# Kernel tuning notes

Measured on AMD Instinct MI355X. Metric: run time of the kernel, lower is better.

## Reference

```python
import jax, jax.numpy as jnp
import numpy as np

# Dims: T timesteps, B batch, C channels, HID expert hidden, E experts, K top-k
T, B, C, HID, E, K, H, W = 4, 8, 256, 1024, 8, 2, 14, 14
EPS = 1e-5       # BatchNorm eps
ALPHA = 4.0      # spikingjelly sigmoid surrogate alpha
V_TH = 1.0       # LIF threshold (spikingjelly default), v_reset = 0.0


@jax.custom_vjp
def spike_fn(u):
    # Heaviside forward, sigmoid-surrogate backward (spikingjelly surrogate.Sigmoid)
    return (u >= 0.0).astype(u.dtype)

def _spike_fwd(u):
    return (u >= 0.0).astype(u.dtype), u

def _spike_bwd(u, g):
    s = jax.nn.sigmoid(ALPHA * u)
    return (g * ALPHA * s * (1.0 - s),)

spike_fn.defvjp(_spike_fwd, _spike_bwd)


def lif(x, tau):
    """MultiStepLIFNode with hard reset (v_reset=0), detach_reset=True.
    x: (T, B, C, H, W) -> spikes of same shape."""
    def step(v, xt):
        h = v + (xt - v) / tau                      # charge
        s = spike_fn(h - V_TH)                      # fire
        v_new = h * (1.0 - jax.lax.stop_gradient(s))  # hard reset, detached spike
        return v_new, s
    _, spikes = jax.lax.scan(step, jnp.zeros_like(x[0]), x)
    return spikes


def conv1x1(x, w, b):
    # x: (T,B,Cin,H,W), w: (Cout,Cin), b: (Cout,) -- 1x1 conv == channel GEMM
    return jnp.einsum('tbchw,oc->tbohw', x, w) + b[None, None, :, None, None]


def bn(x, g, b, m, v, axis):
    # inference-mode BatchNorm with running stats, per-channel on `axis`
    shp = [1] * x.ndim
    shp[axis] = -1
    scale = g.reshape(shp) / jnp.sqrt(v.reshape(shp) + EPS)
    return (x - m.reshape(shp)) * scale + b.reshape(shp)


def expert(x, tau, w1, b1, g1, be1, m1, v1, w2, b2, g2, be2, m2, v2):
    # MS_MLP_Expert.forward: lif -> conv1x1 -> bn -> lif -> conv1x1 -> bn (no residual)
    s1 = lif(x, tau)
    h = bn(conv1x1(s1, w1, b1), g1, be1, m1, v1, axis=2)  # (T,B,HID,H,W)
    s2 = lif(h, tau)
    return bn(conv1x1(s2, w2, b2), g2, be2, m2, v2, axis=2)  # (T,B,C,H,W)


def setup_inputs() -> dict:
    key = jax.random.key(0)
    ks = jax.random.split(key, 16)
    d = {}
    d['x'] = jax.random.normal(ks[0], (T, B, C, H, W), jnp.float32)
    # router (Conv2d(C, E, 1) + BatchNorm2d(E))
    d['router_w'] = jax.random.normal(ks[1], (E, C), jnp.float32) / np.sqrt(C)
    d['router_b'] = jax.random.normal(ks[2], (E,), jnp.float32) * 0.01
    d['rbn_g'] = 1.0 + 0.1 * jax.random.normal(ks[3], (E,), jnp.float32)
    d['rbn_b'] = 0.1 * jax.random.normal(ks[4], (E,), jnp.float32)
    d['rbn_m'] = 0.1 * jax.random.normal(ks[5], (E,), jnp.float32)
    d['rbn_v'] = jax.random.uniform(ks[6], (E,), jnp.float32, 0.5, 1.5)
    # stacked expert params (leading expert axis E)
    d['fc1_w'] = jax.random.normal(ks[7], (E, HID, C), jnp.float32) / np.sqrt(C)
    d['fc1_b'] = 0.01 * jax.random.normal(ks[8], (E, HID), jnp.float32)
    d['bn1_g'] = 1.0 + 0.1 * jax.random.normal(ks[9], (E, HID), jnp.float32)
    d['bn1_b'] = 0.1 * jax.random.normal(ks[10], (E, HID), jnp.float32)
    d['bn1_m'] = 0.1 * jax.random.normal(ks[11], (E, HID), jnp.float32)
    d['bn1_v'] = jax.random.uniform(ks[12], (E, HID), jnp.float32, 0.5, 1.5)
    d['fc2_w'] = jax.random.normal(ks[13], (E, C, HID), jnp.float32) / np.sqrt(HID)
    d['fc2_b'] = 0.01 * jax.random.normal(ks[14], (E, C), jnp.float32)
    d['bn2_g'] = 1.0 + 0.1 * jax.random.normal(ks[15], (E, C), jnp.float32)
    k2 = jax.random.split(jax.random.fold_in(key, 1), 3)
    d['bn2_b'] = 0.1 * jax.random.normal(k2[0], (E, C), jnp.float32)
    d['bn2_m'] = 0.1 * jax.random.normal(k2[1], (E, C), jnp.float32)
    d['bn2_v'] = jax.random.uniform(k2[2], (E, C), jnp.float32, 0.5, 1.5)
    # expert taus: linspace(tau_min=1.5, tau_max=4.0, num_experts)
    d['taus'] = jnp.linspace(1.5, 4.0, E, dtype=jnp.float32)
    return d


def reference(x, router_w, router_b, rbn_g, rbn_b, rbn_m, rbn_v,
              fc1_w, fc1_b, bn1_g, bn1_b, bn1_m, bn1_v,
              fc2_w, fc2_b, bn2_g, bn2_b, bn2_m, bn2_v, taus):
    b_sz = x.shape[1]
    # ---- TemporalRouter ----
    xm = x.mean(axis=0)                                           # (B,C,H,W)
    r = jnp.einsum('bchw,ec->behw', xm, router_w) + router_b[None, :, None, None]
    r = bn(r, rbn_g, rbn_b, rbn_m, rbn_v, axis=1)
    logits = r.mean(axis=(-2, -1))                                # (B,E)
    probs = jax.nn.softmax(logits, axis=-1)
    topw, topi = jax.lax.top_k(probs, K)                          # (B,K)
    topw = topw / topw.sum(axis=-1, keepdims=True)
    # dense combine weights (B,E): top-k entries, 0 elsewhere; detached as in torch
    Wd = jnp.zeros((b_sz, E), x.dtype).at[jnp.arange(b_sz)[:, None], topi].add(topw)
    Wd = jax.lax.stop_gradient(Wd)
    # ---- Experts (dense dispatch: each expert over full batch, masked combine) ----
    outs = jax.vmap(expert, in_axes=(None,) + (0,) * 13)(
        x, taus, fc1_w, fc1_b, bn1_g, bn1_b, bn1_m, bn1_v,
        fc2_w, fc2_b, bn2_g, bn2_b, bn2_m, bn2_v)                 # (E,T,B,C,H,W)
    moe = jnp.einsum('etbchw,be->tbchw', outs, Wd)
    return x + moe
```

## Files before the change

kernel.cpp:

```cpp
#include <hip/hip_runtime.h>
#include <hip/hip_bf16.h>
#include <math.h>

#define T_ 4
#define B_ 8
#define C_ 256
#define HID_ 1024
#define E_ 8
#define HW_ 196
#define M_ 784
#define NPAIR_ 16
#define EPS_ 1e-5f
#define NOUT_ (T_*B_*C_*HW_)

typedef __attribute__((ext_vector_type(8))) short bf16x8;
typedef __attribute__((ext_vector_type(4))) unsigned short u16x4;
typedef __attribute__((ext_vector_type(4))) float f32x4;

__device__ inline unsigned short f2bf(float f){
  union { float f; unsigned u; } v; v.f = f;
  unsigned u = v.u;
  unsigned r = u + 0x7FFFu + ((u >> 16) & 1u);
  return (unsigned short)(r >> 16);
}
__device__ inline float bf2f(unsigned short h){
  union { unsigned u; float f; } v; v.u = ((unsigned)h) << 16;
  return v.f;
}

__device__ inline void gl16(const void* g, void* l){
  auto gp = reinterpret_cast<const unsigned int __attribute__((address_space(1)))*>(
      reinterpret_cast<uintptr_t>(g));
  auto lp = reinterpret_cast<unsigned int __attribute__((address_space(3)))*>(
      reinterpret_cast<uintptr_t>(l));
  __builtin_amdgcn_global_load_lds(gp, lp, 16, 0, 0);
}

__global__ __launch_bounds__(256) void wconv_kernel(
    const float* __restrict__ w1, const float* __restrict__ w2,
    unsigned short* __restrict__ w1h, unsigned short* __restrict__ w1l,
    unsigned short* __restrict__ w2h){
  int i = blockIdx.x * 256 + threadIdx.x;
  float4 v = ((const float4*)w1)[i];
  u16x4 h, l;
  h[0]=f2bf(v.x); l[0]=f2bf(v.x - bf2f(h[0]));
  h[1]=f2bf(v.y); l[1]=f2bf(v.y - bf2f(h[1]));
  h[2]=f2bf(v.z); l[2]=f2bf(v.z - bf2f(h[2]));
  h[3]=f2bf(v.w); l[3]=f2bf(v.w - bf2f(h[3]));
  ((u16x4*)w1h)[i] = h; ((u16x4*)w1l)[i] = l;
  float4 u = ((const float4*)w2)[i];
  u16x4 h2;
  h2[0]=f2bf(u.x); h2[1]=f2bf(u.y); h2[2]=f2bf(u.z); h2[3]=f2bf(u.w);
  ((u16x4*)w2h)[i] = h2;
}

__global__ __launch_bounds__(64) void xbar_kernel(const float* __restrict__ x,
                                                  float* __restrict__ xbar){
  int bc = blockIdx.x;
  int l = threadIdx.x;
  float s = 0.f;
  for (int t = 0; t < T_; t++){
    const float* p = x + ((size_t)(t * B_ * C_) + bc) * HW_;
    for (int i = l; i < HW_; i += 64) s += p[i];
  }
  for (int off = 32; off > 0; off >>= 1) s += __shfl_down(s, off, 64);
  if (l == 0) xbar[bc] = s * (1.0f / (T_ * HW_));
}

__global__ __launch_bounds__(64) void router_kernel(const float* __restrict__ xbar,
    const float* __restrict__ rw, const float* __restrict__ rb,
    const float* __restrict__ rg, const float* __restrict__ rbb,
    const float* __restrict__ rm, const float* __restrict__ rv,
    int* __restrict__ sel_e, float* __restrict__ sel_w){
  __shared__ float lg[64];
  const int tid = threadIdx.x;
  const int b = tid >> 3, e = tid & 7;
  float dot = 0.f;
  for (int c = 0; c < C_; c++) dot += xbar[b * C_ + c] * rw[e * C_ + c];
  dot += rb[e];
  float sc = rg[e] / sqrtf(rv[e] + EPS_);
  lg[tid] = (dot - rm[e]) * sc + rbb[e];
  __syncthreads();
  if (e == 0){
    float l[E_], mx = -1e30f;
    for (int i = 0; i < E_; i++){ l[i] = lg[b * 8 + i]; mx = fmaxf(mx, l[i]); }
    float p[E_];
    for (int i = 0; i < E_; i++) p[i] = expf(l[i] - mx);
    int i1 = 0;
    for (int i = 1; i < E_; i++) if (p[i] > p[i1]) i1 = i;
    int i2 = (i1 == 0) ? 1 : 0;
    for (int i = 0; i < E_; i++) if (i != i1 && p[i] > p[i2]) i2 = i;
    float denom = p[i1] + p[i2];
    sel_e[b * 2]     = i1; sel_w[b * 2]     = p[i1] / denom;
    sel_e[b * 2 + 1] = i2; sel_w[b * 2 + 1] = p[i2] / denom;
  }
}

__global__ __launch_bounds__(256) void lif1_kernel(const float* __restrict__ x,
    const int* __restrict__ sel_e, const float* __restrict__ taus,
    unsigned short* __restrict__ s1){
  const int hw = blockIdx.x;
  const int pair = blockIdx.y;
  const int c = threadIdx.x;
  const int b = pair >> 1;
  const float tau = taus[sel_e[pair]];
  float v = 0.f;
  #pragma unroll
  for (int t = 0; t < T_; t++){
    float xv = x[((size_t)(t * B_ + b) * C_ + c) * HW_ + hw];
    float h = v + (xv - v) / tau;
    float s = (h >= 1.0f) ? 1.0f : 0.0f;
    v = h * (1.0f - s);
    s1[((size_t)pair * M_ + hw * 4 + t) * C_ + c] =
        (s > 0.5f) ? (unsigned short)0x3F80 : (unsigned short)0;
  }
}


__global__ __launch_bounds__(256) void g1_kernel(
    const unsigned short* __restrict__ s1,
    const unsigned short* __restrict__ w1h, const unsigned short* __restrict__ w1l,
    const float* __restrict__ fc1_b,
    const float* __restrict__ bn1_g, const float* __restrict__ bn1_b,
    const float* __restrict__ bn1_m, const float* __restrict__ bn1_v,
    const int* __restrict__ sel_e, const float* __restrict__ taus,
    unsigned short* __restrict__ s2)
{
  __shared__ __align__(16) unsigned short lA[4][2048];
  __shared__ __align__(16) unsigned short lBh[4][2048];
  __shared__ __align__(16) unsigned short lBl[4][2048];
  const int nt = blockIdx.x, mt = blockIdx.y, pair = blockIdx.z;
  const int e = sel_e[pair];
  const int m0 = mt * 64, n0 = nt * 64;
  const int tid = threadIdx.x, lane = tid & 63, wv = tid >> 6;
  const int l15 = lane & 15;
  const int koffs = ((((lane >> 4) ^ (l15 & 3) ^ ((l15 >> 2) & 1)) & 3) << 3);
  const int srow = wv * 16 + (lane >> 2);
  const int scol = ((((lane & 3) ^ ((lane >> 2) & 3) ^ ((lane >> 4) & 1)) & 3) << 3);
  int arow = m0 + srow; if (arow > M_ - 1) arow = M_ - 1;
  const unsigned short* aG  = s1  + ((size_t)pair * M_ + arow) * C_ + scol;
  const unsigned short* bhG = w1h + ((size_t)e * HID_ + n0 + srow) * C_ + scol;
  const unsigned short* blG = w1l + ((size_t)e * HID_ + n0 + srow) * C_ + scol;
  const int lb = wv * 512;
  #pragma unroll
  for (int p = 0; p < 3; p++){
    gl16(aG  + p * 32, &lA[p][lb]);
    gl16(bhG + p * 32, &lBh[p][lb]);
    gl16(blG + p * 32, &lBl[p][lb]);
  }
  f32x4 acc[4] = {};
  #pragma unroll
  for (int kk = 0; kk < 8; kk++){
    if (kk < 6)       asm volatile("s_waitcnt vmcnt(6)" ::: "memory");
    else if (kk == 6) asm volatile("s_waitcnt vmcnt(3)" ::: "memory");
    else              asm volatile("s_waitcnt vmcnt(0)" ::: "memory");
    __builtin_amdgcn_s_barrier();
    __builtin_amdgcn_sched_barrier(0);
    const int cur = kk & 3;
    bf16x8 a = *(const bf16x8*)(&lA[cur][(wv * 16 + l15) * 32 + koffs]);
    #pragma unroll
    for (int cb = 0; cb < 4; cb++){
      bf16x8 bh = *(const bf16x8*)(&lBh[cur][(cb * 16 + l15) * 32 + koffs]);
      bf16x8 bl = *(const bf16x8*)(&lBl[cur][(cb * 16 + l15) * 32 + koffs]);
      acc[cb] = __builtin_amdgcn_mfma_f32_16x16x32_bf16(a, bh, acc[cb], 0, 0, 0);
      acc[cb] = __builtin_amdgcn_mfma_f32_16x16x32_bf16(a, bl, acc[cb], 0, 0, 0);
    }
    if (kk < 5){
      const int nb = (kk + 3) & 3;
      gl16(aG  + (kk + 3) * 32, &lA[nb][lb]);
      gl16(bhG + (kk + 3) * 32, &lBh[nb][lb]);
      gl16(blG + (kk + 3) * 32, &lBl[nb][lb]);
    }
  }
  const float tau = taus[e];
  const int rbase = m0 + wv * 16 + ((lane >> 4) << 2);
  if (rbase < M_){
    #pragma unroll
    for (int cb = 0; cb < 4; cb++){
      int col = n0 + cb * 16 + l15;
      int pi = e * HID_ + col;
      float sc = bn1_g[pi] / sqrtf(bn1_v[pi] + EPS_);
      float mm = bn1_m[pi], bb = bn1_b[pi], cbias = fc1_b[pi];
      float v = 0.f;
      #pragma unroll
      for (int t = 0; t < 4; t++){
        float z = acc[cb][t] + cbias;
        float hin = (z - mm) * sc + bb;
        float h = v + (hin - v) / tau;
        float s = (h >= 1.0f) ? 1.0f : 0.0f;
        v = h * (1.0f - s);
        s2[((size_t)pair * M_ + rbase + t) * HID_ + col] =
            (s > 0.5f) ? (unsigned short)0x3F80 : (unsigned short)0;
      }
    }
  }
}

__global__ __launch_bounds__(256) void g2_kernel(
    const unsigned short* __restrict__ s2,
    const unsigned short* __restrict__ w2h,
    const float* __restrict__ fc2_b,
    const float* __restrict__ bn2_g, const float* __restrict__ bn2_b,
    const float* __restrict__ bn2_m, const float* __restrict__ bn2_v,
    const int* __restrict__ sel_e, const float* __restrict__ sel_w,
    float* __restrict__ y)
{
  __shared__ __align__(16) unsigned short lA[4][2048];
  __shared__ __align__(16) unsigned short lBh[4][2048];
  const int nt = blockIdx.x, mt = blockIdx.y, pair = blockIdx.z;
  const int e = sel_e[pair];
  const float wgt = sel_w[pair];
  const int b = pair >> 1, slot = pair & 1;
  const int m0 = mt * 64, n0 = nt * 64;
  const int tid = threadIdx.x, lane = tid & 63, wv = tid >> 6;
  const int l15 = lane & 15;
  const int koffs = ((((lane >> 4) ^ (l15 & 3) ^ ((l15 >> 2) & 1)) & 3) << 3);
  const int srow = wv * 16 + (lane >> 2);
  const int scol = ((((lane & 3) ^ ((lane >> 2) & 3) ^ ((lane >> 4) & 1)) & 3) << 3);
  int arow = m0 + srow; if (arow > M_ - 1) arow = M_ - 1;
  const unsigned short* aG  = s2  + ((size_t)pair * M_ + arow) * HID_ + scol;
  const unsigned short* bhG = w2h + ((size_t)e * C_ + n0 + srow) * HID_ + scol;
  const int lb = wv * 512;
  #pragma unroll
  for (int p = 0; p < 3; p++){
    gl16(aG  + p * 32, &lA[p][lb]);
    gl16(bhG + p * 32, &lBh[p][lb]);
  }
  f32x4 acc[4] = {};
  #pragma unroll
  for (int kk = 0; kk < 32; kk++){
    if (kk < 30)       asm volatile("s_waitcnt vmcnt(4)" ::: "memory");
    else if (kk == 30) asm volatile("s_waitcnt vmcnt(2)" ::: "memory");
    else               asm volatile("s_waitcnt vmcnt(0)" ::: "memory");
    __builtin_amdgcn_s_barrier();
    __builtin_amdgcn_sched_barrier(0);
    const int cur = kk & 3;
    bf16x8 a = *(const bf16x8*)(&lA[cur][(wv * 16 + l15) * 32 + koffs]);
    #pragma unroll
    for (int cb = 0; cb < 4; cb++){
      bf16x8 bh = *(const bf16x8*)(&lBh[cur][(cb * 16 + l15) * 32 + koffs]);
      acc[cb] = __builtin_amdgcn_mfma_f32_16x16x32_bf16(a, bh, acc[cb], 0, 0, 0);
    }
    if (kk < 29){
      const int nb = (kk + 3) & 3;
      gl16(aG  + (kk + 3) * 32, &lA[nb][lb]);
      gl16(bhG + (kk + 3) * 32, &lBh[nb][lb]);
    }
  }
  const int rbase = m0 + wv * 16 + ((lane >> 4) << 2);
  if (rbase < M_){
    const int hw = rbase >> 2;
    #pragma unroll
    for (int cb = 0; cb < 4; cb++){
      int col = n0 + cb * 16 + l15;
      int pi = e * C_ + col;
      float sc = bn2_g[pi] / sqrtf(bn2_v[pi] + EPS_);
      float mm = bn2_m[pi], bb = bn2_b[pi], cbias = fc2_b[pi];
      #pragma unroll
      for (int t = 0; t < 4; t++){
        float z = acc[cb][t] + cbias;
        float yv = (z - mm) * sc + bb;
        y[(((size_t)slot * T_ + t) * B_ + b) * (C_ * HW_) + (size_t)col * HW_ + hw] =
            wgt * yv;
      }
    }
  }
}

__global__ __launch_bounds__(256) void combine_kernel(const float* __restrict__ x,
    const float* __restrict__ y, float* __restrict__ out){
  int i = blockIdx.x * 256 + threadIdx.x;
  float4 a  = ((const float4*)x)[i];
  float4 b0 = ((const float4*)y)[i];
  float4 b1 = ((const float4*)y)[i + NOUT_ / 4];
  float4 r;
  r.x = a.x + b0.x + b1.x;
  r.y = a.y + b0.y + b1.y;
  r.z = a.z + b0.z + b1.z;
  r.w = a.w + b0.w + b1.w;
  ((float4*)out)[i] = r;
}

extern "C" void kernel_launch(void* const* d_in, const int* in_sizes, int n_in,
                              void* d_out, int out_size, void* d_ws, size_t ws_size,
                              hipStream_t stream){
  const float* x     = (const float*)d_in[0];
  const float* rw    = (const float*)d_in[1];
  const float* rb    = (const float*)d_in[2];
  const float* rg    = (const float*)d_in[3];
  const float* rbb   = (const float*)d_in[4];
  const float* rm    = (const float*)d_in[5];
  const float* rv    = (const float*)d_in[6];
  const float* fc1_w = (const float*)d_in[7];
  const float* fc1_b = (const float*)d_in[8];
  const float* bn1_g = (const float*)d_in[9];
  const float* bn1_b = (const float*)d_in[10];
  const float* bn1_m = (const float*)d_in[11];
  const float* bn1_v = (const float*)d_in[12];
  const float* fc2_w = (const float*)d_in[13];
  const float* fc2_b = (const float*)d_in[14];
  const float* bn2_g = (const float*)d_in[15];
  const float* bn2_b = (const float*)d_in[16];
  const float* bn2_m = (const float*)d_in[17];
  const float* bn2_v = (const float*)d_in[18];
  const float* taus  = (const float*)d_in[19];
  float* out = (float*)d_out;

  char* ws = (char*)d_ws;
  size_t off = 0;
  auto alloc = [&](size_t bytes) -> char* {
    char* p = ws + off;
    off = (off + bytes + 255) & ~(size_t)255;
    return p;
  };
  const int NW = E_ * HID_ * C_;
  unsigned short* s2  = (unsigned short*)alloc((size_t)NPAIR_ * M_ * HID_ * 2);
  unsigned short* w2h = (unsigned short*)alloc((size_t)NW * 2);
  unsigned short* w1h = (unsigned short*)alloc((size_t)NW * 2);
  unsigned short* w1l = (unsigned short*)alloc((size_t)NW * 2);
  unsigned short* s1  = (unsigned short*)alloc((size_t)NPAIR_ * M_ * C_ * 2);
  float* xbar  = (float*)alloc(B_ * C_ * 4);
  int*   sel_e = (int*)alloc(NPAIR_ * 4);
  float* sel_w = (float*)alloc(NPAIR_ * 4);
  float* y = (float*)w1h;
  (void)ws_size; (void)in_sizes; (void)n_in; (void)out_size;

  wconv_kernel<<<NW / 4 / 256, 256, 0, stream>>>(fc1_w, fc2_w, w1h, w1l, w2h);
  xbar_kernel<<<B_ * C_, 64, 0, stream>>>(x, xbar);
  router_kernel<<<1, 64, 0, stream>>>(xbar, rw, rb, rg, rbb, rm, rv, sel_e, sel_w);
  lif1_kernel<<<dim3(HW_, NPAIR_), 256, 0, stream>>>(x, sel_e, taus, s1);
  g1_kernel<<<dim3(HID_ / 64, (M_ + 63) / 64, NPAIR_), 256, 0, stream>>>(
      s1, w1h, w1l, fc1_b, bn1_g, bn1_b, bn1_m, bn1_v, sel_e, taus, s2);
  g2_kernel<<<dim3(C_ / 64, (M_ + 63) / 64, NPAIR_), 256, 0, stream>>>(
      s2, w2h, fc2_b, bn2_g, bn2_b, bn2_m, bn2_v, sel_e, sel_w, y);
  combine_kernel<<<NOUT_ / 4 / 256, 256, 0, stream>>>(x, y, out);
}
```

Baseline: 197.8 us.

## Fuse expert combine and residual into g2, merge prep kernels, coalesce LIF1

```diff
diff --git a/kernel.cpp b/kernel.cpp
--- a/kernel.cpp
+++ b/kernel.cpp
@@ -36,35 +36,38 @@
   __builtin_amdgcn_global_load_lds(gp, lp, 16, 0, 0);
 }
 
-__global__ __launch_bounds__(256) void wconv_kernel(
+__global__ __launch_bounds__(256) void prep_kernel(
     const float* __restrict__ w1, const float* __restrict__ w2,
+    const float* __restrict__ x,
     unsigned short* __restrict__ w1h, unsigned short* __restrict__ w1l,
-    unsigned short* __restrict__ w2h){
-  int i = blockIdx.x * 256 + threadIdx.x;
-  float4 v = ((const float4*)w1)[i];
-  u16x4 h, l;
-  h[0]=f2bf(v.x); l[0]=f2bf(v.x - bf2f(h[0]));
-  h[1]=f2bf(v.y); l[1]=f2bf(v.y - bf2f(h[1]));
-  h[2]=f2bf(v.z); l[2]=f2bf(v.z - bf2f(h[2]));
-  h[3]=f2bf(v.w); l[3]=f2bf(v.w - bf2f(h[3]));
-  ((u16x4*)w1h)[i] = h; ((u16x4*)w1l)[i] = l;
-  float4 u = ((const float4*)w2)[i];
-  u16x4 h2;
-  h2[0]=f2bf(u.x); h2[1]=f2bf(u.y); h2[2]=f2bf(u.z); h2[3]=f2bf(u.w);
-  ((u16x4*)w2h)[i] = h2;
-}
-
-__global__ __launch_bounds__(64) void xbar_kernel(const float* __restrict__ x,
-                                                  float* __restrict__ xbar){
-  int bc = blockIdx.x;
-  int l = threadIdx.x;
-  float s = 0.f;
-  for (int t = 0; t < T_; t++){
-    const float* p = x + ((size_t)(t * B_ * C_) + bc) * HW_;
-    for (int i = l; i < HW_; i += 64) s += p[i];
-  }
-  for (int off = 32; off > 0; off >>= 1) s += __shfl_down(s, off, 64);
-  if (l == 0) xbar[bc] = s * (1.0f / (T_ * HW_));
+    unsigned short* __restrict__ w2h, float* __restrict__ xbar){
+  const int blk = blockIdx.x;
+  if (blk < 2048){
+    int i = blk * 256 + threadIdx.x;
+    float4 v = ((const float4*)w1)[i];
+    u16x4 h, l;
+    h[0]=f2bf(v.x); l[0]=f2bf(v.x - bf2f(h[0]));
+    h[1]=f2bf(v.y); l[1]=f2bf(v.y - bf2f(h[1]));
+    h[2]=f2bf(v.z); l[2]=f2bf(v.z - bf2f(h[2]));
+    h[3]=f2bf(v.w); l[3]=f2bf(v.w - bf2f(h[3]));
+    ((u16x4*)w1h)[i] = h; ((u16x4*)w1l)[i] = l;
+    float4 u = ((const float4*)w2)[i];
+    u16x4 h2;
+    h2[0]=f2bf(u.x); h2[1]=f2bf(u.y); h2[2]=f2bf(u.z); h2[3]=f2bf(u.w);
+    ((u16x4*)w2h)[i] = h2;
+  } else {
+    const int q = blk - 2048;
+    const int g = threadIdx.x >> 6;
+    const int lane = threadIdx.x & 63;
+    const int bc = q * 4 + g;
+    float s = 0.f;
+    for (int t = 0; t < T_; t++){
+      const float* p = x + ((size_t)(t * B_ * C_) + bc) * HW_;
+      for (int i = lane; i < HW_; i += 64) s += p[i];
+    }
+    for (int off = 32; off > 0; off >>= 1) s += __shfl_down(s, off, 64);
+    if (lane == 0) xbar[bc] = s * (1.0f / (T_ * HW_));
+  }
 }
 
 __global__ __launch_bounds__(64) void router_kernel(const float* __restrict__ xbar,
@@ -99,20 +102,20 @@
 __global__ __launch_bounds__(256) void lif1_kernel(const float* __restrict__ x,
     const int* __restrict__ sel_e, const float* __restrict__ taus,
     unsigned short* __restrict__ s1){
-  const int hw = blockIdx.x;
   const int pair = blockIdx.y;
-  const int c = threadIdx.x;
   const int b = pair >> 1;
+  const int f = blockIdx.x * 256 + threadIdx.x;
+  const int c = f / HW_, hw = f - c * HW_;
   const float tau = taus[sel_e[pair]];
+  unsigned short* o = s1 + (size_t)pair * (M_ * C_) + (size_t)(hw * 4) * C_ + c;
   float v = 0.f;
   #pragma unroll
   for (int t = 0; t < T_; t++){
-    float xv = x[((size_t)(t * B_ + b) * C_ + c) * HW_ + hw];
+    float xv = x[(size_t)(t * B_ + b) * (C_ * HW_) + f];
     float h = v + (xv - v) / tau;
     float s = (h >= 1.0f) ? 1.0f : 0.0f;
     v = h * (1.0f - s);
-    s1[((size_t)pair * M_ + hw * 4 + t) * C_ + c] =
-        (s > 0.5f) ? (unsigned short)0x3F80 : (unsigned short)0;
+    o[t * C_] = (s > 0.5f) ? (unsigned short)0x3F80 : (unsigned short)0;
   }
 }
 
@@ -203,14 +206,11 @@
     const float* __restrict__ bn2_g, const float* __restrict__ bn2_b,
     const float* __restrict__ bn2_m, const float* __restrict__ bn2_v,
     const int* __restrict__ sel_e, const float* __restrict__ sel_w,
-    float* __restrict__ y)
+    const float* __restrict__ x, float* __restrict__ out)
 {
   __shared__ __align__(16) unsigned short lA[4][2048];
   __shared__ __align__(16) unsigned short lBh[4][2048];
-  const int nt = blockIdx.x, mt = blockIdx.y, pair = blockIdx.z;
-  const int e = sel_e[pair];
-  const float wgt = sel_w[pair];
-  const int b = pair >> 1, slot = pair & 1;
+  const int nt = blockIdx.x, mt = blockIdx.y, b = blockIdx.z;
   const int m0 = mt * 64, n0 = nt * 64;
   const int tid = threadIdx.x, lane = tid & 63, wv = tid >> 6;
   const int l15 = lane & 15;
@@ -218,38 +218,40 @@
   const int srow = wv * 16 + (lane >> 2);
   const int scol = ((((lane & 3) ^ ((lane >> 2) & 3) ^ ((lane >> 4) & 1)) & 3) << 3);
   int arow = m0 + srow; if (arow > M_ - 1) arow = M_ - 1;
-  const unsigned short* aG  = s2  + ((size_t)pair * M_ + arow) * HID_ + scol;
-  const unsigned short* bhG = w2h + ((size_t)e * C_ + n0 + srow) * HID_ + scol;
   const int lb = wv * 512;
-  #pragma unroll
-  for (int p = 0; p < 3; p++){
-    gl16(aG  + p * 32, &lA[p][lb]);
-    gl16(bhG + p * 32, &lBh[p][lb]);
-  }
-  f32x4 acc[4] = {};
-  #pragma unroll
-  for (int kk = 0; kk < 32; kk++){
-    if (kk < 30)       asm volatile("s_waitcnt vmcnt(4)" ::: "memory");
-    else if (kk == 30) asm volatile("s_waitcnt vmcnt(2)" ::: "memory");
-    else               asm volatile("s_waitcnt vmcnt(0)" ::: "memory");
-    __builtin_amdgcn_s_barrier();
-    __builtin_amdgcn_sched_barrier(0);
-    const int cur = kk & 3;
-    bf16x8 a = *(const bf16x8*)(&lA[cur][(wv * 16 + l15) * 32 + koffs]);
-    #pragma unroll
-    for (int cb = 0; cb < 4; cb++){
-      bf16x8 bh = *(const bf16x8*)(&lBh[cur][(cb * 16 + l15) * 32 + koffs]);
-      acc[cb] = __builtin_amdgcn_mfma_f32_16x16x32_bf16(a, bh, acc[cb], 0, 0, 0);
-    }
-    if (kk < 29){
-      const int nb = (kk + 3) & 3;
-      gl16(aG  + (kk + 3) * 32, &lA[nb][lb]);
-      gl16(bhG + (kk + 3) * 32, &lBh[nb][lb]);
-    }
-  }
-  const int rbase = m0 + wv * 16 + ((lane >> 4) << 2);
-  if (rbase < M_){
-    const int hw = rbase >> 2;
+  f32x4 res[4] = {};
+  for (int slot = 0; slot < 2; slot++){
+    const int pair = b * 2 + slot;
+    const int e = sel_e[pair];
+    const float wgt = sel_w[pair];
+    const unsigned short* aG  = s2  + ((size_t)pair * M_ + arow) * HID_ + scol;
+    const unsigned short* bhG = w2h + ((size_t)e * C_ + n0 + srow) * HID_ + scol;
+    #pragma unroll
+    for (int p = 0; p < 3; p++){
+      gl16(aG  + p * 32, &lA[p][lb]);
+      gl16(bhG + p * 32, &lBh[p][lb]);
+    }
+    f32x4 acc[4] = {};
+    #pragma unroll
+    for (int kk = 0; kk < 32; kk++){
+      if (kk < 30)       asm volatile("s_waitcnt vmcnt(4)" ::: "memory");
+      else if (kk == 30) asm volatile("s_waitcnt vmcnt(2)" ::: "memory");
+      else               asm volatile("s_waitcnt vmcnt(0)" ::: "memory");
+      __builtin_amdgcn_s_barrier();
+      __builtin_amdgcn_sched_barrier(0);
+      const int cur = kk & 3;
+      bf16x8 a = *(const bf16x8*)(&lA[cur][(wv * 16 + l15) * 32 + koffs]);
+      #pragma unroll
+      for (int cb = 0; cb < 4; cb++){
+        bf16x8 bh = *(const bf16x8*)(&lBh[cur][(cb * 16 + l15) * 32 + koffs]);
+        acc[cb] = __builtin_amdgcn_mfma_f32_16x16x32_bf16(a, bh, acc[cb], 0, 0, 0);
+      }
+      if (kk < 29){
+        const int nb = (kk + 3) & 3;
+        gl16(aG  + (kk + 3) * 32, &lA[nb][lb]);
+        gl16(bhG + (kk + 3) * 32, &lBh[nb][lb]);
+      }
+    }
     #pragma unroll
     for (int cb = 0; cb < 4; cb++){
       int col = n0 + cb * 16 + l15;
@@ -259,26 +261,24 @@
       #pragma unroll
       for (int t = 0; t < 4; t++){
         float z = acc[cb][t] + cbias;
-        float yv = (z - mm) * sc + bb;
-        y[(((size_t)slot * T_ + t) * B_ + b) * (C_ * HW_) + (size_t)col * HW_ + hw] =
-            wgt * yv;
-      }
-    }
-  }
-}
-
-__global__ __launch_bounds__(256) void combine_kernel(const float* __restrict__ x,
-    const float* __restrict__ y, float* __restrict__ out){
-  int i = blockIdx.x * 256 + threadIdx.x;
-  float4 a  = ((const float4*)x)[i];
-  float4 b0 = ((const float4*)y)[i];
-  float4 b1 = ((const float4*)y)[i + NOUT_ / 4];
-  float4 r;
-  r.x = a.x + b0.x + b1.x;
-  r.y = a.y + b0.y + b1.y;
-  r.z = a.z + b0.z + b1.z;
-  r.w = a.w + b0.w + b1.w;
-  ((float4*)out)[i] = r;
+        res[cb][t] += wgt * ((z - mm) * sc + bb);
+      }
+    }
+    __syncthreads();
+  }
+  const int rbase = m0 + wv * 16 + ((lane >> 4) << 2);
+  if (rbase < M_){
+    const int hw = rbase >> 2;
+    #pragma unroll
+    for (int cb = 0; cb < 4; cb++){
+      int col = n0 + cb * 16 + l15;
+      #pragma unroll
+      for (int t = 0; t < 4; t++){
+        size_t oi = ((size_t)(t * B_ + b) * C_ + col) * HW_ + hw;
+        out[oi] = x[oi] + res[cb][t];
+      }
+    }
+  }
 }
 
 extern "C" void kernel_launch(void* const* d_in, const int* in_sizes, int n_in,
@@ -322,16 +322,13 @@
   float* xbar  = (float*)alloc(B_ * C_ * 4);
   int*   sel_e = (int*)alloc(NPAIR_ * 4);
   float* sel_w = (float*)alloc(NPAIR_ * 4);
-  float* y = (float*)w1h;
   (void)ws_size; (void)in_sizes; (void)n_in; (void)out_size;
 
-  wconv_kernel<<<NW / 4 / 256, 256, 0, stream>>>(fc1_w, fc2_w, w1h, w1l, w2h);
-  xbar_kernel<<<B_ * C_, 64, 0, stream>>>(x, xbar);
+  prep_kernel<<<2560, 256, 0, stream>>>(fc1_w, fc2_w, x, w1h, w1l, w2h, xbar);
   router_kernel<<<1, 64, 0, stream>>>(xbar, rw, rb, rg, rbb, rm, rv, sel_e, sel_w);
-  lif1_kernel<<<dim3(HW_, NPAIR_), 256, 0, stream>>>(x, sel_e, taus, s1);
+  lif1_kernel<<<dim3((C_ * HW_) / 256, NPAIR_), 256, 0, stream>>>(x, sel_e, taus, s1);
   g1_kernel<<<dim3(HID_ / 64, (M_ + 63) / 64, NPAIR_), 256, 0, stream>>>(
       s1, w1h, w1l, fc1_b, bn1_g, bn1_b, bn1_m, bn1_v, sel_e, taus, s2);
-  g2_kernel<<<dim3(C_ / 64, (M_ + 63) / 64, NPAIR_), 256, 0, stream>>>(
-      s2, w2h, fc2_b, bn2_g, bn2_b, bn2_m, bn2_v, sel_e, sel_w, y);
-  combine_kernel<<<NOUT_ / 4 / 256, 256, 0, stream>>>(x, y, out);
-}
+  g2_kernel<<<dim3(C_ / 64, (M_ + 63) / 64, B_), 256, 0, stream>>>(
+      s2, w2h, fc2_b, bn2_g, bn2_b, bn2_m, bn2_v, sel_e, sel_w, x, out);
+}
```

New measurement: 193.9 us. About the same (-1.9%).
